# Kernel optimization log

Measured on AMD Instinct MI355X. Metric: run time of the kernel, lower is better.

## Reference

```python
import jax, jax.numpy as jnp
import numpy as np

B, N, M = 4, 8192, 8192


def setup_inputs() -> dict:
    key = jax.random.key(0)
    k1, k2 = jax.random.split(key)
    xyz1 = jax.random.normal(k1, (B, N, 3), dtype=jnp.float32)
    xyz2 = jax.random.normal(k2, (B, M, 3), dtype=jnp.float32)
    return {"xyz1": xyz1, "xyz2": xyz2}


def _chamfer(xyz1, xyz2):
    # Squared Euclidean pairwise distances via the expansion
    # ||a-b||^2 = ||a||^2 + ||b||^2 - 2 a.b  (avoids a [B,N,M,3] diff tensor).
    sq1 = jnp.sum(xyz1 * xyz1, axis=-1)              # [B,N]
    sq2 = jnp.sum(xyz2 * xyz2, axis=-1)              # [B,M]
    inner = jnp.einsum('bnd,bmd->bnm', xyz1, xyz2)   # [B,N,M]
    d = sq1[:, :, None] + sq2[:, None, :] - 2.0 * inner
    d = jnp.maximum(d, 0.0)
    dist1 = jnp.min(d, axis=2)  # [B,N] nearest xyz2 point for each xyz1 point
    dist2 = jnp.min(d, axis=1)  # [B,M] nearest xyz1 point for each xyz2 point
    return dist1, dist2


def reference(xyz1, xyz2):
    return _chamfer(xyz1, xyz2)
```

## Files before the change

### kernel.cpp

```cpp
#include <hip/hip_runtime.h>


typedef __bf16 bf16_t;
typedef __bf16 bf16x8 __attribute__((ext_vector_type(8)));
typedef float  f32x16 __attribute__((ext_vector_type(16)));

#define NPTS    8192
#define NB      4
#define NSETPTS (NB * NPTS)
#define TPB     256
#define WAVES   4
#define QPW     2
#define QC      (WAVES * QPW * 32)
#define QPANELS (NPTS / QC)
#define SEGR    8
#define RC      (NPTS / SEGR)
#define RT      (RC / 32)
#define NSLOT   (RC * 2)

__global__ void chamfer_init_out(unsigned int* __restrict__ out, int n) {
    int i = blockIdx.x * blockDim.x + threadIdx.x;
    if (i < n) out[i] = 0x7F800000u;
}

__device__ __forceinline__ void gload16(const bf16_t* g, bf16_t* l) {
    __builtin_amdgcn_global_load_lds(
        (const __attribute__((address_space(1))) void*)g,
        (__attribute__((address_space(3))) void*)l, 16, 0, 0);
}

__device__ __forceinline__ void split2(float v, bf16_t& h, bf16_t& l) {
    h = (bf16_t)v;
    l = (bf16_t)(v - (float)h);
}

__device__ __forceinline__ float tree16(const f32x16& x) {
    float a0 = fminf(x[0],  x[1]);
    float a1 = fminf(x[2],  x[3]);
    float a2 = fminf(x[4],  x[5]);
    float a3 = fminf(x[6],  x[7]);
    float a4 = fminf(x[8],  x[9]);
    float a5 = fminf(x[10], x[11]);
    float a6 = fminf(x[12], x[13]);
    float a7 = fminf(x[14], x[15]);
    a0 = fminf(a0, a1); a2 = fminf(a2, a3);
    a4 = fminf(a4, a5); a6 = fminf(a6, a7);
    return fminf(fminf(a0, a2), fminf(a4, a6));
}

__global__ void chamfer_prep(const float* __restrict__ xyz1,
                             const float* __restrict__ xyz2,
                             bf16_t* __restrict__ a16,
                             bf16_t* __restrict__ b16) {
    int i = blockIdx.x * blockDim.x + threadIdx.x;
    const int perm[16] = {0,1,2,3, 8,9,10,11, 4,5,6,7, 12,13,14,15};

    {
        float x = xyz1[3 * i], y = xyz1[3 * i + 1], z = xyz1[3 * i + 2];
        float sq = x * x + y * y + z * z;
        bf16_t m2xh, m2xl, m2yh, m2yl, m2zh, m2zl, sqh, sql;
        split2(-2.f * x, m2xh, m2xl);
        split2(-2.f * y, m2yh, m2yl);
        split2(-2.f * z, m2zh, m2zl);
        split2(sq, sqh, sql);
        bf16_t one = (bf16_t)1.0f, zero = (bf16_t)0.0f;
        bf16_t A[16] = { m2xh, m2yh, m2zh,  m2xl, m2yl, m2zl,
                         m2xh, m2yh, m2zh,  sqh, sql, one, one, zero, zero, zero };
        bf16_t* ao = a16 + (size_t)i * 16;
#pragma unroll
        for (int j = 0; j < 16; ++j) ao[j] = A[perm[j]];
    }

    {
        float x = xyz2[3 * i], y = xyz2[3 * i + 1], z = xyz2[3 * i + 2];
        float sq = x * x + y * y + z * z;
        bf16_t xh, xl, yh, yl, zh, zl, sqh, sql;
        split2(x, xh, xl);
        split2(y, yh, yl);
        split2(z, zh, zl);
        split2(sq, sqh, sql);
        bf16_t one = (bf16_t)1.0f, zero = (bf16_t)0.0f;
        bf16_t Bv[16] = { xh, yh, zh,  xh, yh, zh,  xl, yl, zl,
                          one, one, sqh, sql, zero, zero, zero };
        int p = i & 31;
        size_t tb = (size_t)(i & ~31) * 16;
        int s0 = (2 * p)     ^ (p & 7);
        int s1 = (2 * p + 1) ^ (p & 7);
        bf16_t* bo0 = b16 + tb + (size_t)s0 * 8;
        bf16_t* bo1 = b16 + tb + (size_t)s1 * 8;
#pragma unroll
        for (int j = 0; j < 8; ++j) bo0[j] = Bv[perm[j]];
#pragma unroll
        for (int j = 0; j < 8; ++j) bo1[j] = Bv[perm[j + 8]];
    }
}

__global__ __launch_bounds__(TPB, 4) void chamfer_main(
    const bf16_t* __restrict__ a16,
    const bf16_t* __restrict__ b16,
    unsigned int* __restrict__ out)
{
    __shared__ __align__(16) unsigned char smem[NSLOT * 16];
    __shared__ unsigned int colmin[RC];
    bf16_t* sbuf = (bf16_t*)smem;
    float (*red)[32][33] = (float (*)[32][33])smem;

    int bid = blockIdx.x;
    int s   = bid & (SEGR - 1);    bid >>= 3;
    int qp  = bid & (QPANELS - 1); bid >>= 5;
    int b   = bid;

    int wave = threadIdx.x >> 6;
    int lane = threadIdx.x & 63;
    int col  = lane & 31;
    int h    = lane >> 5;

    const bf16_t* ap = a16 + (size_t)b * NPTS * 16;
    const bf16_t* gB = b16 + (size_t)(b * NPTS + s * RC) * 16;

#pragma unroll
    for (int c = 0; c < 8; ++c) {
        int slot = c * 256 + threadIdx.x;
        gload16(gB + (size_t)slot * 8, sbuf + (size_t)slot * 8);
    }

#pragma unroll
    for (int k = 0; k < RC / TPB; ++k)
        colmin[k * TPB + threadIdx.x] = 0x7F800000u;

    int qbase = qp * QC + wave * (QPW * 32);
    bf16x8 af0 = *((const bf16x8*)(ap + (size_t)(qbase +  0 + col) * 16) + h);
    bf16x8 af1 = *((const bf16x8*)(ap + (size_t)(qbase + 32 + col) * 16) + h);

    f32x16 rm0, rm1, zacc;
#pragma unroll
    for (int g = 0; g < 16; ++g) {
        rm0[g] = INFINITY; rm1[g] = INFINITY; zacc[g] = 0.f;
    }

    __syncthreads();

    int swz = ((2 * col + h) ^ (col & 7)) * 8;
    const bf16_t* sl = sbuf + swz;

#pragma unroll 1
    for (int t = 0; t < RT; t += 2) {
        bf16x8 c0 = *(const bf16x8*)(sl + (size_t)(t + 0) * 512);
        bf16x8 c1 = *(const bf16x8*)(sl + (size_t)(t + 1) * 512);

        f32x16 x0 = __builtin_amdgcn_mfma_f32_32x32x16_bf16(af0, c0, zacc, 0, 0, 0);
        f32x16 x1 = __builtin_amdgcn_mfma_f32_32x32x16_bf16(af0, c1, zacc, 0, 0, 0);
#pragma unroll
        for (int g = 0; g < 16; ++g) rm0[g] = fminf(fminf(x0[g], x1[g]), rm0[g]);
        float s0 = tree16(x0);
        float s1 = tree16(x1);

        f32x16 x2 = __builtin_amdgcn_mfma_f32_32x32x16_bf16(af1, c0, zacc, 0, 0, 0);
        f32x16 x3 = __builtin_amdgcn_mfma_f32_32x32x16_bf16(af1, c1, zacc, 0, 0, 0);
#pragma unroll
        for (int g = 0; g < 16; ++g) rm1[g] = fminf(fminf(x2[g], x3[g]), rm1[g]);
        float s2 = tree16(x2);
        float s3 = tree16(x3);

        float m0 = fminf(s0, s2);
        float m1 = fminf(s1, s3);
        m0 = fminf(m0, __shfl_xor(m0, 32));
        m1 = fminf(m1, __shfl_xor(m1, 32));
        m0 = fmaxf(m0, 0.f);
        m1 = fmaxf(m1, 0.f);
        if (h == 0) {
            atomicMin(&colmin[t * 32 + col],       __float_as_uint(m0));
            atomicMin(&colmin[(t + 1) * 32 + col], __float_as_uint(m1));
        }
    }

    __syncthreads();

    {
        int out2base = NSETPTS + b * NPTS + s * RC;
#pragma unroll
        for (int k = 0; k < RC / TPB; ++k) {
            int j = k * TPB + threadIdx.x;
            atomicMin(&out[out2base + j], colmin[j]);
        }
    }

    int outbase = b * NPTS + qp * QC;

#define RED_PASS(QT, RM)                                                      \
    {                                                                         \
        _Pragma("unroll")                                                     \
        for (int g = 0; g < 16; ++g) {                                        \
            int row = (g & 3) + 8 * (g >> 2) + 4 * h;                         \
            red[wave][row][col] = RM[g];                                      \
        }                                                                     \
        __syncthreads();                                                      \
        if (threadIdx.x < 128) {                                              \
            int w = threadIdx.x >> 5, r = threadIdx.x & 31;                   \
            const float* rp = &red[w][r][0];                                  \
            float v0 = rp[0], v1 = rp[1], v2 = rp[2], v3 = rp[3];             \
            _Pragma("unroll")                                                 \
            for (int cc = 4; cc < 32; cc += 4) {                              \
                v0 = fminf(v0, rp[cc + 0]);                                   \
                v1 = fminf(v1, rp[cc + 1]);                                   \
                v2 = fminf(v2, rp[cc + 2]);                                   \
                v3 = fminf(v3, rp[cc + 3]);                                   \
            }                                                                 \
            float v = fmaxf(fminf(fminf(v0, v1), fminf(v2, v3)), 0.f);        \
            atomicMin(&out[outbase + w * (QPW * 32) + (QT) * 32 + r],         \
                      __float_as_uint(v));                                    \
        }                                                                     \
        __syncthreads();                                                      \
    }

    RED_PASS(0, rm0)
    RED_PASS(1, rm1)
#undef RED_PASS
}

extern "C" void kernel_launch(void* const* d_in, const int* in_sizes, int n_in,
                              void* d_out, int out_size, void* d_ws, size_t ws_size,
                              hipStream_t stream) {
    const float* xyz1 = (const float*)d_in[0];
    const float* xyz2 = (const float*)d_in[1];
    unsigned int* out = (unsigned int*)d_out;

    bf16_t* a16 = (bf16_t*)d_ws;
    bf16_t* b16 = a16 + (size_t)NSETPTS * 16;

    hipLaunchKernelGGL(chamfer_init_out,
                       dim3((out_size + TPB - 1) / TPB), dim3(TPB), 0, stream,
                       out, out_size);

    hipLaunchKernelGGL(chamfer_prep,
                       dim3(NSETPTS / TPB), dim3(TPB), 0, stream,
                       xyz1, xyz2, a16, b16);

    hipLaunchKernelGGL(chamfer_main,
                       dim3(NB * QPANELS * SEGR), dim3(TPB), 0, stream,
                       a16, b16, out);
}
```

Before: 79.72 us.

## Drop per-wave query tiling to one 32-row tile and split references into 16 segments

```diff
diff --git a/kernel.cpp b/kernel.cpp
--- a/kernel.cpp
+++ b/kernel.cpp
@@ -10,10 +10,9 @@
 #define NSETPTS (NB * NPTS)
 #define TPB     256
 #define WAVES   4
-#define QPW     2
-#define QC      (WAVES * QPW * 32)
+#define QC      (WAVES * 32)
 #define QPANELS (NPTS / QC)
-#define SEGR    8
+#define SEGR    16
 #define RC      (NPTS / SEGR)
 #define RT      (RC / 32)
 #define NSLOT   (RC * 2)
@@ -35,17 +34,14 @@
 }
 
 __device__ __forceinline__ float tree16(const f32x16& x) {
-    float a0 = fminf(x[0],  x[1]);
-    float a1 = fminf(x[2],  x[3]);
-    float a2 = fminf(x[4],  x[5]);
-    float a3 = fminf(x[6],  x[7]);
-    float a4 = fminf(x[8],  x[9]);
-    float a5 = fminf(x[10], x[11]);
-    float a6 = fminf(x[12], x[13]);
-    float a7 = fminf(x[14], x[15]);
-    a0 = fminf(a0, a1); a2 = fminf(a2, a3);
-    a4 = fminf(a4, a5); a6 = fminf(a6, a7);
-    return fminf(fminf(a0, a2), fminf(a4, a6));
+    float a = fminf(fminf(x[0],  x[1]),  x[2]);
+    float b = fminf(fminf(x[3],  x[4]),  x[5]);
+    float c = fminf(fminf(x[6],  x[7]),  x[8]);
+    float d = fminf(fminf(x[9],  x[10]), x[11]);
+    float e = fminf(fminf(x[12], x[13]), x[14]);
+    a = fminf(fminf(a, b), x[15]);
+    c = fminf(fminf(c, d), e);
+    return fminf(a, c);
 }
 
 __global__ void chamfer_prep(const float* __restrict__ xyz1,
@@ -95,19 +91,19 @@
     }
 }
 
-__global__ __launch_bounds__(TPB, 4) void chamfer_main(
+__global__ __launch_bounds__(TPB) void chamfer_main(
     const bf16_t* __restrict__ a16,
     const bf16_t* __restrict__ b16,
     unsigned int* __restrict__ out)
 {
-    __shared__ __align__(16) unsigned char smem[NSLOT * 16];
+    __shared__ __align__(16) unsigned char smem[WAVES * 32 * 33 * 4];
     __shared__ unsigned int colmin[RC];
     bf16_t* sbuf = (bf16_t*)smem;
     float (*red)[32][33] = (float (*)[32][33])smem;
 
     int bid = blockIdx.x;
-    int s   = bid & (SEGR - 1);    bid >>= 3;
-    int qp  = bid & (QPANELS - 1); bid >>= 5;
+    int s   = bid & (SEGR - 1);    bid >>= 4;
+    int qp  = bid & (QPANELS - 1); bid >>= 6;
     int b   = bid;
 
     int wave = threadIdx.x >> 6;
@@ -119,7 +115,7 @@
     const bf16_t* gB = b16 + (size_t)(b * NPTS + s * RC) * 16;
 
 #pragma unroll
-    for (int c = 0; c < 8; ++c) {
+    for (int c = 0; c < 4; ++c) {
         int slot = c * 256 + threadIdx.x;
         gload16(gB + (size_t)slot * 8, sbuf + (size_t)slot * 8);
     }
@@ -128,15 +124,12 @@
     for (int k = 0; k < RC / TPB; ++k)
         colmin[k * TPB + threadIdx.x] = 0x7F800000u;
 
-    int qbase = qp * QC + wave * (QPW * 32);
-    bf16x8 af0 = *((const bf16x8*)(ap + (size_t)(qbase +  0 + col) * 16) + h);
-    bf16x8 af1 = *((const bf16x8*)(ap + (size_t)(qbase + 32 + col) * 16) + h);
-
-    f32x16 rm0, rm1, zacc;
-#pragma unroll
-    for (int g = 0; g < 16; ++g) {
-        rm0[g] = INFINITY; rm1[g] = INFINITY; zacc[g] = 0.f;
-    }
+    int qbase = qp * QC + wave * 32;
+    bf16x8 af = *((const bf16x8*)(ap + (size_t)(qbase + col) * 16) + h);
+
+    f32x16 rm, zacc;
+#pragma unroll
+    for (int g = 0; g < 16; ++g) { rm[g] = INFINITY; zacc[g] = 0.f; }
 
     __syncthreads();
 
@@ -148,24 +141,16 @@
         bf16x8 c0 = *(const bf16x8*)(sl + (size_t)(t + 0) * 512);
         bf16x8 c1 = *(const bf16x8*)(sl + (size_t)(t + 1) * 512);
 
-        f32x16 x0 = __builtin_amdgcn_mfma_f32_32x32x16_bf16(af0, c0, zacc, 0, 0, 0);
-        f32x16 x1 = __builtin_amdgcn_mfma_f32_32x32x16_bf16(af0, c1, zacc, 0, 0, 0);
-#pragma unroll
-        for (int g = 0; g < 16; ++g) rm0[g] = fminf(fminf(x0[g], x1[g]), rm0[g]);
+        f32x16 x0 = __builtin_amdgcn_mfma_f32_32x32x16_bf16(af, c0, zacc, 0, 0, 0);
+        f32x16 x1 = __builtin_amdgcn_mfma_f32_32x32x16_bf16(af, c1, zacc, 0, 0, 0);
+
+#pragma unroll
+        for (int g = 0; g < 16; ++g) rm[g] = fminf(fminf(x0[g], x1[g]), rm[g]);
+
         float s0 = tree16(x0);
         float s1 = tree16(x1);
-
-        f32x16 x2 = __builtin_amdgcn_mfma_f32_32x32x16_bf16(af1, c0, zacc, 0, 0, 0);
-        f32x16 x3 = __builtin_amdgcn_mfma_f32_32x32x16_bf16(af1, c1, zacc, 0, 0, 0);
-#pragma unroll
-        for (int g = 0; g < 16; ++g) rm1[g] = fminf(fminf(x2[g], x3[g]), rm1[g]);
-        float s2 = tree16(x2);
-        float s3 = tree16(x3);
-
-        float m0 = fminf(s0, s2);
-        float m1 = fminf(s1, s3);
-        m0 = fminf(m0, __shfl_xor(m0, 32));
-        m1 = fminf(m1, __shfl_xor(m1, 32));
+        float m0 = fminf(s0, __shfl_xor(s0, 32));
+        float m1 = fminf(s1, __shfl_xor(s1, 32));
         m0 = fmaxf(m0, 0.f);
         m1 = fmaxf(m1, 0.f);
         if (h == 0) {
@@ -185,37 +170,27 @@
         }
     }
 
-    int outbase = b * NPTS + qp * QC;
-
-#define RED_PASS(QT, RM)                                                      \
-    {                                                                         \
-        _Pragma("unroll")                                                     \
-        for (int g = 0; g < 16; ++g) {                                        \
-            int row = (g & 3) + 8 * (g >> 2) + 4 * h;                         \
-            red[wave][row][col] = RM[g];                                      \
-        }                                                                     \
-        __syncthreads();                                                      \
-        if (threadIdx.x < 128) {                                              \
-            int w = threadIdx.x >> 5, r = threadIdx.x & 31;                   \
-            const float* rp = &red[w][r][0];                                  \
-            float v0 = rp[0], v1 = rp[1], v2 = rp[2], v3 = rp[3];             \
-            _Pragma("unroll")                                                 \
-            for (int cc = 4; cc < 32; cc += 4) {                              \
-                v0 = fminf(v0, rp[cc + 0]);                                   \
-                v1 = fminf(v1, rp[cc + 1]);                                   \
-                v2 = fminf(v2, rp[cc + 2]);                                   \
-                v3 = fminf(v3, rp[cc + 3]);                                   \
-            }                                                                 \
-            float v = fmaxf(fminf(fminf(v0, v1), fminf(v2, v3)), 0.f);        \
-            atomicMin(&out[outbase + w * (QPW * 32) + (QT) * 32 + r],         \
-                      __float_as_uint(v));                                    \
-        }                                                                     \
-        __syncthreads();                                                      \
-    }
-
-    RED_PASS(0, rm0)
-    RED_PASS(1, rm1)
-#undef RED_PASS
+#pragma unroll
+    for (int g = 0; g < 16; ++g) {
+        int row = (g & 3) + 8 * (g >> 2) + 4 * h;
+        red[wave][row][col] = rm[g];
+    }
+    __syncthreads();
+
+    if (threadIdx.x < QC) {
+        int w = threadIdx.x >> 5, r = threadIdx.x & 31;
+        const float* rp = &red[w][r][0];
+        float v0 = rp[0], v1 = rp[1], v2 = rp[2], v3 = rp[3];
+#pragma unroll
+        for (int cc = 4; cc < 32; cc += 4) {
+            v0 = fminf(v0, rp[cc + 0]);
+            v1 = fminf(v1, rp[cc + 1]);
+            v2 = fminf(v2, rp[cc + 2]);
+            v3 = fminf(v3, rp[cc + 3]);
+        }
+        float v = fmaxf(fminf(fminf(v0, v1), fminf(v2, v3)), 0.f);
+        atomicMin(&out[b * NPTS + qp * QC + threadIdx.x], __float_as_uint(v));
+    }
 }
 
 extern "C" void kernel_launch(void* const* d_in, const int* in_sizes, int n_in,
```

Result: no change. 79.44 us (-0.4%).
